# Kernel tuning notes

Measured on AMD Instinct MI355X. Metric: run time of the kernel, lower is better.

Reference implementation:

```python
import jax, jax.numpy as jnp
import numpy as np

M = 100   # memory_size
D = 512   # memory_dim
B, C, H, W = 4, 512, 64, 64
LN_EPS = 512.0  # nn.LayerNorm(300, 512): 2nd positional arg is eps (faithful quirk)


def _l2norm(x):
    # F.normalize(x, dim=1): x / max(||x||_2, 1e-12)
    return x / jnp.maximum(jnp.linalg.norm(x, axis=1, keepdims=True), 1e-12)


def setup_inputs() -> dict:
    key = jax.random.key(0)
    ks = jax.random.split(key, 16)
    s = 0.03  # weight scale to keep activations sane
    return {
        "fea":    jax.random.normal(ks[0], (B, C, H, W), jnp.float32),
        "item_w": jax.random.normal(ks[1], (D, D), jnp.float32) * 0.02,
        "rel_w":  jax.random.normal(ks[2], (M, D, D), jnp.float32) * 0.02,
        "W1": jax.random.normal(ks[3], (C, D), jnp.float32) * s,  "b1": jnp.zeros((D,), jnp.float32),
        "W2": jax.random.normal(ks[4], (C, D), jnp.float32) * s,  "b2": jnp.zeros((D,), jnp.float32),
        "W3": jax.random.normal(ks[5], (C, M), jnp.float32) * s,  "b3": jnp.zeros((M,), jnp.float32),
        "Wqkv": jax.random.normal(ks[6], (D, 3 * M), jnp.float32) * s, "bqkv": jnp.zeros((3 * M,), jnp.float32),
        "ln_g": jnp.ones((3 * M,), jnp.float32), "ln_b": jnp.zeros((3 * M,), jnp.float32),
        "Wr1": jax.random.normal(ks[7], (D * D, D), jnp.float32) * s, "br1": jnp.zeros((D,), jnp.float32),
        "Wr2": jax.random.normal(ks[8], (M * D, D), jnp.float32) * s, "br2": jnp.zeros((D,), jnp.float32),
    }


def reference(fea, item_w, rel_w, W1, b1, W2, b2, W3, b3,
              Wqkv, bqkv, ln_g, ln_b, Wr1, br1, Wr2, br2):
    b, c, h, w = fea.shape
    x = fea.transpose(0, 2, 3, 1).reshape(b * h * w, c)        # (N, C)
    qn = _l2norm(x)
    ip1 = qn @ W1 + b1                                          # (N, D)
    ip2 = qn @ W2 + b2                                          # (N, D)
    ip3 = jax.nn.softmax(qn @ W3 + b3, axis=-1)                 # (N, M)
    # ip4[b,f] = sum_{n,d} ip3[b,n] ip2[b,d] rel_w[n,d,f]; scan over the M
    # memory slots to avoid an (N, M, D) intermediate.
    def _slot(acc, nw):
        coef, Wn = nw                                           # (N,), (D, D)
        return acc + coef[:, None] * (ip2 @ Wn), None
    ip4, _ = jax.lax.scan(_slot, jnp.zeros_like(ip2), (ip3.T, rel_w))
    # einsum('bd,cf->df', ip4, ip2) == outer(sum_b ip4, sum_c ip2)
    item0 = jnp.outer(ip4.sum(0), ip2.sum(0))                   # (D, D)
    item1 = item_w + ip1.T @ ip1                                # (D, D)
    qkv = (item0 + 1.0 * item1) @ Wqkv + bqkv                   # alpha2=1.0, (D, 3M)
    mu = qkv.mean(-1, keepdims=True)
    var = jnp.var(qkv, axis=-1, keepdims=True)                  # biased, as torch LN
    qkv = (qkv - mu) / jnp.sqrt(var + LN_EPS) * ln_g + ln_b
    q, k, v = qkv[:, :M].T, qkv[:, M:2 * M].T, qkv[:, 2 * M:].T  # each (M, D)
    # op_att: rel0[i,d,f] = sum_j tanh(q[i,d]*k[j,d]) * v[j,f]
    t = jnp.tanh(q[:, None, :] * k[None, :, :])                 # (M, M, D)
    rel0 = jnp.einsum('ijd,jf->idf', t, v)                      # (M, D, D)
    rel_w_new = rel_w + 1.0 * rel0                              # alpha1=1.0
    memory = rel_w_new.reshape(M, D * D) @ Wr1 + br1            # (M, D)
    mn = _l2norm(memory)
    addr = jax.nn.softmax(qn @ mn.T, axis=1)                    # (N, M)
    mf = (addr @ mn).reshape(b, h, w, c).transpose(0, 3, 1, 2)  # (b, C, h, w)
    return jnp.concatenate([fea, mf], axis=1)                   # (b, 2C, h, w)
```

## Files before the change

### kernel.cpp

```cpp
#include <hip/hip_runtime.h>
#include <hip/hip_bf16.h>

#define NTOK 16384
#define DDIM 512
#define MMEM 100
#define HWSZ 4096
#define QKVW 300

typedef __attribute__((ext_vector_type(8))) short short8v;
typedef __attribute__((ext_vector_type(4))) short short4v;
typedef __attribute__((ext_vector_type(4))) float f32x4;

__device__ __forceinline__ unsigned short f2bf(float x) {
  union { __hip_bfloat16 h; unsigned short u; } cv;
  cv.h = __float2bfloat16(x);
  return cv.u;
}
__device__ __forceinline__ float bf2f(unsigned short u) {
  union { unsigned int u; float f; } v; v.u = ((unsigned int)u) << 16;
  return v.f;
}

__global__ __launch_bounds__(256) void feat_cvtw_k(
    const float* __restrict__ fea, unsigned short* __restrict__ qnbf,
    float* __restrict__ out,
    const float* __restrict__ W1, const float* __restrict__ W2,
    const float* __restrict__ W3, const float* __restrict__ Wq,
    const float* __restrict__ b1, const float* __restrict__ b2,
    unsigned short* __restrict__ Wcat, unsigned short* __restrict__ o3,
    unsigned short* __restrict__ oq, float* __restrict__ bcat) {
  if (blockIdx.x >= 512) {
    int base = (blockIdx.x - 512) * 256 + threadIdx.x;
    for (int idx = base; idx < 467968; idx += 229 * 256) {
      if (idx < 262144) {
        int k = idx >> 9, n = idx & 511;
        Wcat[(size_t)k * 1024 + n] = f2bf(W1[idx]);
        Wcat[(size_t)k * 1024 + 512 + n] = f2bf(W2[idx]);
      } else if (idx < 313344) {
        o3[idx - 262144] = f2bf(W3[idx - 262144]);
      } else if (idx < 466944) {
        oq[idx - 313344] = f2bf(Wq[idx - 313344]);
      } else {
        int i = idx - 466944;
        bcat[i] = (i < 512) ? b1[i] : b2[i - 512];
      }
    }
    return;
  }
  __shared__ float tile[512][33];
  __shared__ float psum[8][32];
  __shared__ float invn_s[32];
  const int bid = blockIdx.x;
  const int b = bid >> 7, hw0 = (bid & 127) * 32;
  const int t = threadIdx.x;
  const int hwo = t & 31, cg = t >> 5;
  const float* src = fea + (size_t)b * DDIM * HWSZ + hw0;
  float* dst = out + (size_t)b * (2 * DDIM) * HWSZ + hw0;
  float ss = 0.f;
#pragma unroll 8
  for (int i = 0; i < 64; ++i) {
    int c = cg * 64 + i;
    float v = src[(size_t)c * HWSZ + hwo];
    tile[c][hwo] = v;
    dst[(size_t)c * HWSZ + hwo] = v;
    ss += v * v;
  }
  psum[cg][hwo] = ss;
  __syncthreads();
  if (t < 32) {
    float s = 0.f;
#pragma unroll
    for (int j = 0; j < 8; ++j) s += psum[j][t];
    invn_s[t] = 1.f / fmaxf(sqrtf(s), 1e-12f);
  }
  __syncthreads();
  const int tok = t & 31, c0 = (t >> 5) * 64;
  const float inv = invn_s[tok];
  unsigned short* qp = qnbf + ((size_t)(b * HWSZ + hw0 + tok)) * DDIM + c0;
#pragma unroll
  for (int e8 = 0; e8 < 8; ++e8) {
    short8v p;
#pragma unroll
    for (int e = 0; e < 8; ++e)
      p[e] = (short)f2bf(tile[c0 + e8 * 8 + e][tok] * inv);
    *(short8v*)(qp + e8 * 8) = p;
  }
}

template<bool OUTBF>
__global__ __launch_bounds__(256) void gemm_bf16_k(
    const unsigned short* __restrict__ A, const unsigned short* __restrict__ B,
    const float* __restrict__ bias, void* __restrict__ Cv,
    int M, int N, int K, int lda, int ldb, int ldc) {
  __shared__ unsigned short As[128][40];
  __shared__ unsigned short Bs[32][132];
  const int tid = threadIdx.x;
  const int l = tid & 63, w = tid >> 6;
  const int l15 = l & 15, lhi = l >> 4;
  const int wm = w >> 1, wn = w & 1;
  const int row0 = blockIdx.y * 128, col0 = blockIdx.x * 128;
  const int am = tid >> 1, akq = (tid & 1) << 4;
  const int bk = tid >> 3, bnq = (tid & 7) << 4;
  const int arow = row0 + am;
  f32x4 acc[4][4] = {};

  for (int k0 = 0; k0 < K; k0 += 32) {
    short8v av0 = {}, av1 = {}, bv0 = {}, bv1 = {};
    if (arow < M && k0 + akq < K) {
      const unsigned short* ap = A + (size_t)arow * lda + k0 + akq;
      if (k0 + akq + 15 < K) {
        av0 = *(const short8v*)ap;
        av1 = *(const short8v*)(ap + 8);
      } else {
#pragma unroll
        for (int e = 0; e < 8; ++e) {
          av0[e] = (k0 + akq + e < K) ? (short)ap[e] : (short)0;
          av1[e] = (k0 + akq + 8 + e < K) ? (short)ap[8 + e] : (short)0;
        }
      }
    }
    {
      const int kk = k0 + bk;
      if (kk < K) {
        const unsigned short* bp = B + (size_t)kk * ldb + col0 + bnq;
        if (col0 + bnq + 15 < N) {
          bv0 = *(const short8v*)bp;
          bv1 = *(const short8v*)(bp + 8);
        } else {
#pragma unroll
          for (int e = 0; e < 8; ++e) {
            bv0[e] = (col0 + bnq + e < N) ? (short)bp[e] : (short)0;
            bv1[e] = (col0 + bnq + 8 + e < N) ? (short)bp[8 + e] : (short)0;
          }
        }
      }
    }
    __syncthreads();
    *(short8v*)&As[am][akq] = av0;
    *(short8v*)&As[am][akq + 8] = av1;
    *(short8v*)&Bs[bk][bnq] = bv0;
    *(short8v*)&Bs[bk][bnq + 8] = bv1;
    __syncthreads();
    short8v af[4];
#pragma unroll
    for (int mt = 0; mt < 4; ++mt)
      af[mt] = *(const short8v*)&As[wm * 64 + mt * 16 + l15][lhi * 8];
#pragma unroll
    for (int ct = 0; ct < 4; ++ct) {
      union { short8v v; unsigned short u[8]; } bf;
      const int nn = wn * 64 + ct * 16 + l15;
#pragma unroll
      for (int j = 0; j < 8; ++j) bf.u[j] = Bs[lhi * 8 + j][nn];
#pragma unroll
      for (int mt = 0; mt < 4; ++mt)
        acc[mt][ct] = __builtin_amdgcn_mfma_f32_16x16x32_bf16(
            af[mt], bf.v, acc[mt][ct], 0, 0, 0);
    }
  }

#pragma unroll
  for (int mt = 0; mt < 4; ++mt) {
    const int rb = row0 + wm * 64 + mt * 16 + lhi * 4;
#pragma unroll
    for (int u = 0; u < 4; ++u) {
      const int r = rb + u;
      if (r >= M) continue;
#pragma unroll
      for (int ct = 0; ct < 4; ++ct) {
        const int c = col0 + wn * 64 + ct * 16 + l15;
        if (c >= N) continue;
        float val = acc[mt][ct][u];
        if (bias) val += bias[c];
        if (OUTBF) ((unsigned short*)Cv)[(size_t)r * ldc + c] = f2bf(val);
        else       ((float*)Cv)[(size_t)r * ldc + c] = val;
      }
    }
  }
}

__global__ __launch_bounds__(256) void gemm_qkv_k(
    const float* __restrict__ item, const float* __restrict__ item_w,
    const float* __restrict__ s4, const float* __restrict__ s2,
    const unsigned short* __restrict__ B, const float* __restrict__ bias,
    float* __restrict__ C) {
  __shared__ unsigned short As[128][40];
  __shared__ unsigned short Bs[32][132];
  const int tid = threadIdx.x;
  const int l = tid & 63, w = tid >> 6;
  const int l15 = l & 15, lhi = l >> 4;
  const int wm = w >> 1, wn = w & 1;
  const int row0 = blockIdx.y * 128, col0 = blockIdx.x * 128;
  const int am = tid >> 1, akq = (tid & 1) << 4;
  const int bk = tid >> 3, bnq = (tid & 7) << 4;
  const int arow = row0 + am;
  f32x4 acc[4][4] = {};

  for (int k0 = 0; k0 < DDIM; k0 += 32) {
    float av[16];
    {
      const size_t off = (size_t)arow * DDIM + k0 + akq;
      const float s4r = s4[arow];
#pragma unroll
      for (int u = 0; u < 4; ++u) {
        float4 a = *(const float4*)(item + off + 4 * u);
        float4 b = *(const float4*)(item_w + off + 4 * u);
        float4 c = *(const float4*)(s2 + k0 + akq + 4 * u);
        av[4*u+0] = a.x + b.x + s4r * c.x;
        av[4*u+1] = a.y + b.y + s4r * c.y;
        av[4*u+2] = a.z + b.z + s4r * c.z;
        av[4*u+3] = a.w + b.w + s4r * c.w;
      }
    }
    short8v bv0 = {}, bv1 = {};
    {
      const int kk = k0 + bk;
      const unsigned short* bp = B + (size_t)kk * QKVW + col0 + bnq;
      if (col0 + bnq + 15 < QKVW) {
        bv0 = *(const short8v*)bp;
        bv1 = *(const short8v*)(bp + 8);
      } else {
#pragma unroll
        for (int e = 0; e < 8; ++e) {
          bv0[e] = (col0 + bnq + e < QKVW) ? (short)bp[e] : (short)0;
          bv1[e] = (col0 + bnq + 8 + e < QKVW) ? (short)bp[8 + e] : (short)0;
        }
      }
    }
    __syncthreads();
    {
      short8v p0, p1;
#pragma unroll
      for (int e = 0; e < 8; ++e) p0[e] = (short)f2bf(av[e]);
#pragma unroll
      for (int e = 0; e < 8; ++e) p1[e] = (short)f2bf(av[8 + e]);
      *(short8v*)&As[am][akq] = p0;
      *(short8v*)&As[am][akq + 8] = p1;
    }
    *(short8v*)&Bs[bk][bnq] = bv0;
    *(short8v*)&Bs[bk][bnq + 8] = bv1;
    __syncthreads();
    short8v af[4];
#pragma unroll
    for (int mt = 0; mt < 4; ++mt)
      af[mt] = *(const short8v*)&As[wm * 64 + mt * 16 + l15][lhi * 8];
#pragma unroll
    for (int ct = 0; ct < 4; ++ct) {
      union { short8v v; unsigned short u[8]; } bf;
      const int nn = wn * 64 + ct * 16 + l15;
#pragma unroll
      for (int j = 0; j < 8; ++j) bf.u[j] = Bs[lhi * 8 + j][nn];
#pragma unroll
      for (int mt = 0; mt < 4; ++mt)
        acc[mt][ct] = __builtin_amdgcn_mfma_f32_16x16x32_bf16(
            af[mt], bf.v, acc[mt][ct], 0, 0, 0);
    }
  }

#pragma unroll
  for (int mt = 0; mt < 4; ++mt) {
    const int rb = row0 + wm * 64 + mt * 16 + lhi * 4;
#pragma unroll
    for (int u = 0; u < 4; ++u) {
      const int r = rb + u;
#pragma unroll
      for (int ct = 0; ct < 4; ++ct) {
        const int c = col0 + wn * 64 + ct * 16 + l15;
        if (c >= QKVW) continue;
        C[(size_t)r * QKVW + c] = acc[mt][ct][u] + bias[c];
      }
    }
  }
}

__global__ __launch_bounds__(256) void gemm_sm100_k(
    const unsigned short* __restrict__ A, const unsigned short* __restrict__ B,
    const float* __restrict__ bias, unsigned short* __restrict__ obf,
    int lda, int ldb, int ldo) {
  __shared__ unsigned short As[128][40];
  __shared__ unsigned short Bs[32][132];
  __shared__ float Ps[128][104];
  const int tid = threadIdx.x;
  const int l = tid & 63, w = tid >> 6;
  const int l15 = l & 15, lhi = l >> 4;
  const int wm = w >> 1, wn = w & 1;
  const int row0 = blockIdx.x * 128;
  const int am = tid >> 1, akq = (tid & 1) << 4;
  const int bk = tid >> 3, bnq = (tid & 7) << 4;
  f32x4 acc[4][4] = {};

  for (int k0 = 0; k0 < DDIM; k0 += 32) {
    const unsigned short* ap = A + (size_t)(row0 + am) * lda + k0 + akq;
    short8v av0 = *(const short8v*)ap;
    short8v av1 = *(const short8v*)(ap + 8);
    short8v bv0 = {}, bv1 = {};
    const unsigned short* bp = B + (size_t)(k0 + bk) * ldb + bnq;
    if (bnq + 15 < MMEM) {
      bv0 = *(const short8v*)bp;
      bv1 = *(const short8v*)(bp + 8);
    } else {
#pragma unroll
      for (int e = 0; e < 8; ++e) {
        bv0[e] = (bnq + e < MMEM) ? (short)bp[e] : (short)0;
        bv1[e] = (bnq + 8 + e < MMEM) ? (short)bp[8 + e] : (short)0;
      }
    }
    __syncthreads();
    *(short8v*)&As[am][akq] = av0;
    *(short8v*)&As[am][akq + 8] = av1;
    *(short8v*)&Bs[bk][bnq] = bv0;
    *(short8v*)&Bs[bk][bnq + 8] = bv1;
    __syncthreads();
    short8v af[4];
#pragma unroll
    for (int mt = 0; mt < 4; ++mt)
      af[mt] = *(const short8v*)&As[wm * 64 + mt * 16 + l15][lhi * 8];
#pragma unroll
    for (int ct = 0; ct < 4; ++ct) {
      union { short8v v; unsigned short u[8]; } bf;
      const int nn = wn * 64 + ct * 16 + l15;
#pragma unroll
      for (int j = 0; j < 8; ++j) bf.u[j] = Bs[lhi * 8 + j][nn];
#pragma unroll
      for (int mt = 0; mt < 4; ++mt)
        acc[mt][ct] = __builtin_amdgcn_mfma_f32_16x16x32_bf16(
            af[mt], bf.v, acc[mt][ct], 0, 0, 0);
    }
  }

#pragma unroll
  for (int mt = 0; mt < 4; ++mt) {
#pragma unroll
    for (int u = 0; u < 4; ++u) {
      const int r = wm * 64 + mt * 16 + lhi * 4 + u;
#pragma unroll
      for (int ct = 0; ct < 4; ++ct) {
        const int c = wn * 64 + ct * 16 + l15;
        if (c < MMEM) {
          float val = acc[mt][ct][u];
          if (bias) val += bias[c];
          Ps[r][c] = val;
        }
      }
    }
  }
  __syncthreads();
  for (int rr = 0; rr < 32; ++rr) {
    const int r = w * 32 + rr;
    float v0 = Ps[r][l];
    const bool has1 = (l + 64) < MMEM;
    float v1 = has1 ? Ps[r][l + 64] : -3.4e38f;
    float m = fmaxf(v0, v1);
#pragma unroll
    for (int o = 32; o; o >>= 1) m = fmaxf(m, __shfl_xor(m, o, 64));
    float e0 = expf(v0 - m);
    float e1 = has1 ? expf(v1 - m) : 0.f;
    float s = e0 + e1;
#pragma unroll
    for (int o = 32; o; o >>= 1) s += __shfl_xor(s, o, 64);
    float inv = 1.f / s;
    unsigned short* orow = obf + (size_t)(row0 + r) * ldo;
    orow[l] = f2bf(e0 * inv);
    if (has1) orow[l + 64] = f2bf(e1 * inv);
  }
}

__global__ __launch_bounds__(256) void atb_bf16_k(
    const unsigned short* __restrict__ A, const unsigned short* __restrict__ B,
    float* __restrict__ C, int M, int N, int K,
    int lda, int ldb, int ldc, int KC) {
  __shared__ unsigned short As[128][40];
  __shared__ unsigned short Bs[32][132];
  const int tid = threadIdx.x;
  const int l = tid & 63, w = tid >> 6;
  const int l15 = l & 15, lhi = l >> 4;
  const int wm = w >> 1, wn = w & 1;
  const int row0 = blockIdx.y * 128, col0 = blockIdx.x * 128;
  const int kbeg = blockIdx.z * KC;
  const int kend = min(kbeg + KC, K);
  const int akk = tid >> 3, amq = (tid & 7) << 4;
  const int bk = tid >> 3, bnq = (tid & 7) << 4;
  f32x4 acc[4][4] = {};

  for (int k0 = kbeg; k0 < kend; k0 += 32) {
    unsigned short av[16]; short8v bv0 = {}, bv1 = {};
    {
      const int kk = k0 + akk;
      if (kk < kend) {
        const unsigned short* ap = A + (size_t)kk * lda + row0 + amq;
        if (row0 + amq + 15 < M) {
          *(short8v*)&av[0] = *(const short8v*)ap;
          *(short8v*)&av[8] = *(const short8v*)(ap + 8);
        } else {
#pragma unroll
          for (int e = 0; e < 16; ++e)
            av[e] = (row0 + amq + e < M) ? ap[e] : 0;
        }
      } else {
#pragma unroll
        for (int e = 0; e < 16; ++e) av[e] = 0;
      }
    }
    {
      const int kk = k0 + bk;
      if (kk < kend) {
        const unsigned short* bp = B + (size_t)kk * ldb + col0 + bnq;
        if (col0 + bnq + 15 < N) {
          bv0 = *(const short8v*)bp;
          bv1 = *(const short8v*)(bp + 8);
        } else {
#pragma unroll
          for (int e = 0; e < 8; ++e) {
            bv0[e] = (col0 + bnq + e < N) ? (short)bp[e] : (short)0;
            bv1[e] = (col0 + bnq + 8 + e < N) ? (short)bp[8 + e] : (short)0;
          }
        }
      }
    }
    __syncthreads();
#pragma unroll
    for (int e = 0; e < 16; ++e) As[amq + e][akk] = av[e];
    *(short8v*)&Bs[bk][bnq] = bv0;
    *(short8v*)&Bs[bk][bnq + 8] = bv1;
    __syncthreads();
    short8v af[4];
#pragma unroll
    for (int mt = 0; mt < 4; ++mt)
      af[mt] = *(const short8v*)&As[wm * 64 + mt * 16 + l15][lhi * 8];
#pragma unroll
    for (int ct = 0; ct < 4; ++ct) {
      union { short8v v; unsigned short u[8]; } bf;
      const int nn = wn * 64 + ct * 16 + l15;
#pragma unroll
      for (int j = 0; j < 8; ++j) bf.u[j] = Bs[lhi * 8 + j][nn];
#pragma unroll
      for (int mt = 0; mt < 4; ++mt)
        acc[mt][ct] = __builtin_amdgcn_mfma_f32_16x16x32_bf16(
            af[mt], bf.v, acc[mt][ct], 0, 0, 0);
    }
  }

#pragma unroll
  for (int mt = 0; mt < 4; ++mt) {
    const int rb = row0 + wm * 64 + mt * 16 + lhi * 4;
#pragma unroll
    for (int u = 0; u < 4; ++u) {
      const int r = rb + u;
      if (r >= M) continue;
#pragma unroll
      for (int ct = 0; ct < 4; ++ct) {
        const int c = col0 + wn * 64 + ct * 16 + l15;
        if (c >= N) continue;
        atomicAdd(&C[(size_t)r * ldc + c], acc[mt][ct][u]);
      }
    }
  }
}

__global__ __launch_bounds__(256) void rel0_mfma_k(
    const float* __restrict__ qm, const float* __restrict__ km,
    const float* __restrict__ vm, const float* __restrict__ rel_w,
    unsigned short* __restrict__ relbf) {
  __shared__ unsigned short Ts[128][136];
  __shared__ unsigned short Vs[128][136];
  __shared__ float qv[128];
  const int i = blockIdx.y;
  const int d0 = blockIdx.x * 128;
  const int tid = threadIdx.x;
  const int l = tid & 63, w = tid >> 6;
  const int l15 = l & 15, lhi = l >> 4;
  const int wm = w >> 1, wn = w & 1;

  if (tid < 128) qv[tid] = qm[(size_t)i * DDIM + d0 + tid];
  __syncthreads();
#pragma unroll
  for (int p = 0; p < 8; ++p) {
    int g = p * 2048 + tid * 8;
    int j = g >> 7, dd = g & 127;
    if (j < MMEM) {
      const float* kp = km + (size_t)j * DDIM + d0 + dd;
      float4 k0v = *(const float4*)kp;
      float4 k1v = *(const float4*)(kp + 4);
      float kv[8] = {k0v.x, k0v.y, k0v.z, k0v.w, k1v.x, k1v.y, k1v.z, k1v.w};
#pragma unroll
      for (int e = 0; e < 8; ++e)
        Ts[dd + e][j] = f2bf(tanhf(qv[dd + e] * kv[e]));
    } else {
#pragma unroll
      for (int e = 0; e < 8; ++e) Ts[dd + e][j] = 0;
    }
  }

  for (int f0 = 0; f0 < DDIM; f0 += 128) {
    __syncthreads();
#pragma unroll
    for (int p = 0; p < 8; ++p) {
      int g = p * 2048 + tid * 8;
      int j = g >> 7, ff = g & 127;
      short8v pv;
      if (j < MMEM) {
        const float* vp = vm + (size_t)j * DDIM + f0 + ff;
        float4 v0 = *(const float4*)vp;
        float4 v1 = *(const float4*)(vp + 4);
        pv[0] = (short)f2bf(v0.x); pv[1] = (short)f2bf(v0.y);
        pv[2] = (short)f2bf(v0.z); pv[3] = (short)f2bf(v0.w);
        pv[4] = (short)f2bf(v1.x); pv[5] = (short)f2bf(v1.y);
        pv[6] = (short)f2bf(v1.z); pv[7] = (short)f2bf(v1.w);
      } else {
#pragma unroll
        for (int e = 0; e < 8; ++e) pv[e] = 0;
      }
      *(short8v*)&Vs[j][ff] = pv;
    }
    __syncthreads();
    f32x4 acc[4][4] = {};
#pragma unroll
    for (int ks = 0; ks < 4; ++ks) {
      const int kb = ks * 32;
      short8v af[4];
#pragma unroll
      for (int mt = 0; mt < 4; ++mt)
        af[mt] = *(const short8v*)&Ts[wm * 64 + mt * 16 + l15][kb + lhi * 8];
#pragma unroll
      for (int ct = 0; ct < 4; ++ct) {
        union { short8v v; unsigned short u[8]; } bf;
        const int nn = wn * 64 + ct * 16 + l15;
#pragma unroll
        for (int jj = 0; jj < 8; ++jj) bf.u[jj] = Vs[kb + lhi * 8 + jj][nn];
#pragma unroll
        for (int mt = 0; mt < 4; ++mt)
          acc[mt][ct] = __builtin_amdgcn_mfma_f32_16x16x32_bf16(
              af[mt], bf.v, acc[mt][ct], 0, 0, 0);
      }
    }
#pragma unroll
    for (int mt = 0; mt < 4; ++mt) {
#pragma unroll
      for (int u = 0; u < 4; ++u) {
        const int d = d0 + wm * 64 + mt * 16 + lhi * 4 + u;
        const size_t base = (size_t)i * 262144 + (size_t)d * DDIM;
#pragma unroll
        for (int ct = 0; ct < 4; ++ct) {
          const int f = f0 + wn * 64 + ct * 16 + l15;
          relbf[base + f] = f2bf(rel_w[base + f] + acc[mt][ct][u]);
        }
      }
    }
  }
}

#define MGK 262144
#define MGKC 1024
#define MGCHUNK 256
__global__ __launch_bounds__(1024, 4) void memgemm_k(
    const unsigned short* __restrict__ Ag, const float* __restrict__ Bg,
    float* __restrict__ partial) {
  __shared__ unsigned short As[128][44];
  __shared__ unsigned short Bs[32][520];
  const int tid = threadIdx.x;
  const int l = tid & 63, w = tid >> 6;
  const int l15 = l & 15, lhi = l >> 4;
  const int kbeg = blockIdx.x * MGKC;
  const int arow = tid >> 3, akq = tid & 7;
  const int bk = tid >> 5, bnq = (tid & 31) * 16;
  const int bsw = ((bk >> 3) & 3) << 4;
  const int csw = lhi << 4;
  f32x4 acc[8][2] = {};

  for (int t32 = 0; t32 < MGKC / 32; ++t32) {
    const int kb = kbeg + t32 * 32;
    short4v av = {};
    if (arow < MMEM)
      av = *(const short4v*)(Ag + (size_t)arow * MGK + kb + akq * 4);
    float4 bv[4];
    const float* bp = Bg + (size_t)(kb + bk) * DDIM + bnq;
#pragma unroll
    for (int u = 0; u < 4; ++u) bv[u] = *(const float4*)(bp + 4 * u);
    __syncthreads();
    *(short4v*)&As[arow][akq * 4] = av;
#pragma unroll
    for (int u = 0; u < 2; ++u) {
      short8v pb;
      pb[0] = (short)f2bf(bv[2*u].x);   pb[1] = (short)f2bf(bv[2*u].y);
      pb[2] = (short)f2bf(bv[2*u].z);   pb[3] = (short)f2bf(bv[2*u].w);
      pb[4] = (short)f2bf(bv[2*u+1].x); pb[5] = (short)f2bf(bv[2*u+1].y);
      pb[6] = (short)f2bf(bv[2*u+1].z); pb[7] = (short)f2bf(bv[2*u+1].w);
      *(short8v*)&Bs[bk][(bnq + u * 8) ^ bsw] = pb;
    }
    __syncthreads();
    union { short8v v; unsigned short u[8]; } bf0, bf1;
    const int nn0 = w * 32 + l15, nn1 = w * 32 + 16 + l15;
#pragma unroll
    for (int j = 0; j < 8; ++j) {
      bf0.u[j] = Bs[lhi * 8 + j][nn0 ^ csw];
      bf1.u[j] = Bs[lhi * 8 + j][nn1 ^ csw];
    }
#pragma unroll
    for (int mt = 0; mt < 8; ++mt) {
      short8v af = *(const short8v*)&As[mt * 16 + l15][lhi * 8];
      acc[mt][0] = __builtin_amdgcn_mfma_f32_16x16x32_bf16(af, bf0.v, acc[mt][0], 0, 0, 0);
      acc[mt][1] = __builtin_amdgcn_mfma_f32_16x16x32_bf16(af, bf1.v, acc[mt][1], 0, 0, 0);
    }
  }

  float* pw = partial + (size_t)blockIdx.x * (MMEM * DDIM);
#pragma unroll
  for (int mt = 0; mt < 8; ++mt) {
    const int r0 = mt * 16 + lhi * 4;
#pragma unroll
    for (int r = 0; r < 4; ++r) {
      const int row = r0 + r;
      if (row < MMEM) {
        pw[(size_t)row * DDIM + w * 32 + l15]      = acc[mt][0][r];
        pw[(size_t)row * DDIM + w * 32 + 16 + l15] = acc[mt][1][r];
      }
    }
  }
}

__global__ __launch_bounds__(512) void reduce_mn_k(
    const float* __restrict__ partial, const float* __restrict__ br1,
    unsigned short* __restrict__ mnbf, unsigned short* __restrict__ mnTbf) {
  __shared__ float r1[8];
  const int i = blockIdx.x, t = threadIdx.x;
  const float* p = partial + (size_t)i * DDIM + t;
  float a0 = 0.f, a1 = 0.f, a2 = 0.f, a3 = 0.f;
  float a4 = 0.f, a5 = 0.f, a6 = 0.f, a7 = 0.f;
  const size_t zs = (size_t)(MMEM * DDIM);
  for (int z = 0; z < MGCHUNK; z += 8) {
    a0 += p[(z + 0) * zs]; a1 += p[(z + 1) * zs];
    a2 += p[(z + 2) * zs]; a3 += p[(z + 3) * zs];
    a4 += p[(z + 4) * zs]; a5 += p[(z + 5) * zs];
    a6 += p[(z + 6) * zs]; a7 += p[(z + 7) * zs];
  }
  float a = br1[t] + ((a0 + a1) + (a2 + a3)) + ((a4 + a5) + (a6 + a7));
  float q = a * a;
#pragma unroll
  for (int o = 32; o; o >>= 1) q += __shfl_xor(q, o, 64);
  if ((t & 63) == 0) r1[t >> 6] = q;
  __syncthreads();
  q = 0.f;
#pragma unroll
  for (int j = 0; j < 8; ++j) q += r1[j];
  float inv = 1.f / fmaxf(sqrtf(q), 1e-12f);
  unsigned short hv = f2bf(a * inv);
  mnbf[(size_t)i * DDIM + t] = hv;
  mnTbf[(size_t)t * MMEM + i] = hv;
}

__global__ __launch_bounds__(512) void colsum_bf_k(const unsigned short* __restrict__ A,
                                                   int ld, float* __restrict__ out) {
  int d = threadIdx.x;
  const unsigned short* p = A + (size_t)blockIdx.x * 64 * ld + d;
  float a0 = 0.f, a1 = 0.f, a2 = 0.f, a3 = 0.f;
  for (int r = 0; r < 64; r += 4) {
    a0 += bf2f(p[(size_t)(r + 0) * ld]);
    a1 += bf2f(p[(size_t)(r + 1) * ld]);
    a2 += bf2f(p[(size_t)(r + 2) * ld]);
    a3 += bf2f(p[(size_t)(r + 3) * ld]);
  }
  atomicAdd(&out[d], (a0 + a1) + (a2 + a3));
}

__global__ __launch_bounds__(256) void ip4sum_k(const float* __restrict__ S,
                                                const float* __restrict__ rel_w,
                                                float* __restrict__ out) {
  __shared__ float sv[64];
  int r0 = blockIdx.x * 64;
  int tid = threadIdx.x;
  if (tid < 64) sv[tid] = S[r0 + tid];
  __syncthreads();
  float a0 = 0.f, a1 = 0.f, a2 = 0.f, a3 = 0.f;
  float b0 = 0.f, b1 = 0.f, b2 = 0.f, b3 = 0.f;
  const float* base = rel_w + (size_t)r0 * DDIM;
  for (int r = 0; r < 64; r += 4) {
    const float* p0 = base + (size_t)(r + 0) * DDIM;
    const float* p1 = base + (size_t)(r + 1) * DDIM;
    const float* p2 = base + (size_t)(r + 2) * DDIM;
    const float* p3 = base + (size_t)(r + 3) * DDIM;
    a0 = fmaf(sv[r + 0], p0[tid], a0); b0 = fmaf(sv[r + 0], p0[tid + 256], b0);
    a1 = fmaf(sv[r + 1], p1[tid], a1); b1 = fmaf(sv[r + 1], p1[tid + 256], b1);
    a2 = fmaf(sv[r + 2], p2[tid], a2); b2 = fmaf(sv[r + 2], p2[tid + 256], b2);
    a3 = fmaf(sv[r + 3], p3[tid], a3); b3 = fmaf(sv[r + 3], p3[tid + 256], b3);
  }
  atomicAdd(&out[tid], (a0 + a1) + (a2 + a3));
  atomicAdd(&out[tid + 256], (b0 + b1) + (b2 + b3));
}

__global__ __launch_bounds__(256) void ln300_k(const float* __restrict__ x,
                                               const float* __restrict__ g,
                                               const float* __restrict__ bb,
                                               float* __restrict__ qm,
                                               float* __restrict__ km,
                                               float* __restrict__ vm) {
  __shared__ float r1[4], r2[4];
  int row = blockIdx.x, tid = threadIdx.x;
  const float* xr = x + (size_t)row * QKVW;
  float v1 = xr[tid];
  float v2 = (tid + 256 < QKVW) ? xr[tid + 256] : 0.f;
  float s = v1 + v2, q = v1 * v1 + v2 * v2;
#pragma unroll
  for (int o = 32; o; o >>= 1) { s += __shfl_xor(s, o, 64); q += __shfl_xor(q, o, 64); }
  if ((tid & 63) == 0) { r1[tid >> 6] = s; r2[tid >> 6] = q; }
  __syncthreads();
  s = r1[0] + r1[1] + r1[2] + r1[3];
  q = r2[0] + r2[1] + r2[2] + r2[3];
  float mean = s * (1.f / 300.f);
  float var = q * (1.f / 300.f) - mean * mean;
  float inv = rsqrtf(var + 512.0f);
  float y1 = (v1 - mean) * inv * g[tid] + bb[tid];
  int j = tid;
  if (j < 100)      qm[(size_t)j * DDIM + row] = y1;
  else if (j < 200) km[(size_t)(j - 100) * DDIM + row] = y1;
  else              vm[(size_t)(j - 200) * DDIM + row] = y1;
  if (tid + 256 < QKVW) {
    float y2 = (v2 - mean) * inv * g[tid + 256] + bb[tid + 256];
    vm[(size_t)(tid + 56) * DDIM + row] = y2;
  }
}

__global__ void write_mf_k(const unsigned short* __restrict__ mfbf,
                           float* __restrict__ out) {
  __shared__ float tile[32][33];
  int b = blockIdx.z, hw0 = blockIdx.x * 32, c0 = blockIdx.y * 32;
  int tx = threadIdx.x, ty = threadIdx.y;
#pragma unroll
  for (int i = 0; i < 32; i += 8)
    tile[ty + i][tx] =
        bf2f(mfbf[((size_t)b * HWSZ + hw0 + ty + i) * DDIM + c0 + tx]);
  __syncthreads();
#pragma unroll
  for (int i = 0; i < 32; i += 8)
    out[(size_t)b * 4194304 + (size_t)(512 + c0 + ty + i) * HWSZ + hw0 + tx] =
        tile[tx][ty + i];
}

extern "C" void kernel_launch(void* const* d_in, const int* in_sizes, int n_in,
                              void* d_out, int out_size, void* d_ws, size_t ws_size,
                              hipStream_t stream) {
  (void)in_sizes; (void)n_in; (void)out_size; (void)ws_size;
  const float* fea    = (const float*)d_in[0];
  const float* item_w = (const float*)d_in[1];
  const float* rel_w  = (const float*)d_in[2];
  const float* W1     = (const float*)d_in[3];
  const float* b1     = (const float*)d_in[4];
  const float* W2     = (const float*)d_in[5];
  const float* b2     = (const float*)d_in[6];
  const float* W3     = (const float*)d_in[7];
  const float* b3     = (const float*)d_in[8];
  const float* Wqkv   = (const float*)d_in[9];
  const float* bqkv   = (const float*)d_in[10];
  const float* ln_g   = (const float*)d_in[11];
  const float* ln_b   = (const float*)d_in[12];
  const float* Wr1    = (const float*)d_in[13];
  const float* br1    = (const float*)d_in[14];
  float* out = (float*)d_out;
  float* ws = (float*)d_ws;

  float* S       = ws;
  float* ip4sum  = S       + 51200;
  float* ip2sum  = ip4sum  + 512;
  float* item    = ip2sum  + 512;
  float* qkv     = item    + 262144;
  float* qm      = qkv     + 153600;
  float* km      = qm      + 51200;
  float* vm      = km      + 51200;
  float* bcat    = vm      + 51200;
  float* partial = bcat    + 1024;
  unsigned short* u16base = (unsigned short*)(partial + 13107200);
  unsigned short* qnbf    = u16base;
  unsigned short* ip12bf  = qnbf    + 8388608;
  unsigned short* ip3bf   = ip12bf  + 16777216;
  unsigned short* addrbf  = ip3bf   + 1638400;
  unsigned short* relbf   = addrbf  + 2097152;
  unsigned short* mfbf    = relbf   + 26214400;
  unsigned short* mnbf    = mfbf    + 8388608;
  unsigned short* mnTbf   = mnbf    + 51200;
  unsigned short* Wcat    = mnTbf   + 51200;
  unsigned short* W3bf    = Wcat    + 524288;
  unsigned short* Wqbf    = W3bf    + 51200;

  hipMemsetAsync(S, 0, (size_t)(51200 + 512 + 512 + 262144) * sizeof(float), stream);

  feat_cvtw_k<<<741, 256, 0, stream>>>(fea, qnbf, out, W1, W2, W3, Wqkv,
                                       b1, b2, Wcat, W3bf, Wqbf, bcat);

  gemm_bf16_k<true><<<dim3(8, 128), 256, 0, stream>>>(
      qnbf, Wcat, bcat, ip12bf, NTOK, 1024, DDIM, DDIM, 1024, 1024);
  gemm_sm100_k<<<128, 256, 0, stream>>>(qnbf, W3bf, b3, ip3bf, DDIM, MMEM, MMEM);

  atb_bf16_k<<<dim3(4, 4, 32), 256, 0, stream>>>(
      ip12bf, ip12bf, item, DDIM, DDIM, NTOK, 1024, 1024, DDIM, 512);
  atb_bf16_k<<<dim3(4, 1, 64), 256, 0, stream>>>(
      ip3bf, ip12bf + 512, S, MMEM, DDIM, NTOK, MMEM, 1024, DDIM, 256);
  colsum_bf_k<<<256, 512, 0, stream>>>(ip12bf + 512, 1024, ip2sum);
  ip4sum_k<<<800, 256, 0, stream>>>(S, rel_w, ip4sum);

  gemm_qkv_k<<<dim3(3, 4), 256, 0, stream>>>(item, item_w, ip4sum, ip2sum,
                                             Wqbf, bqkv, qkv);
  ln300_k<<<512, 256, 0, stream>>>(qkv, ln_g, ln_b, qm, km, vm);

  rel0_mfma_k<<<dim3(4, MMEM), 256, 0, stream>>>(qm, km, vm, rel_w, relbf);

  memgemm_k<<<dim3(MGCHUNK), 1024, 0, stream>>>(relbf, Wr1, partial);
  reduce_mn_k<<<MMEM, 512, 0, stream>>>(partial, br1, mnbf, mnTbf);

  gemm_sm100_k<<<128, 256, 0, stream>>>(qnbf, mnTbf, nullptr, addrbf, DDIM, MMEM, 128);
  gemm_bf16_k<true><<<dim3(4, 128), 256, 0, stream>>>(
      addrbf, mnbf, nullptr, mfbf, NTOK, DDIM, MMEM, 128, DDIM, DDIM);

  write_mf_k<<<dim3(128, 16, 4), dim3(32, 8), 0, stream>>>(mfbf, out);
}
```

Measured before the change: 554.4 us.

## Merge independent GEMM launches and fuse mf GEMM with transposed output write

Combines the ip1/ip2 GEMM and the ip3 softmax GEMM into one launch that dispatches on block index. It also merges the two A^T·B reductions and the ip2 column sum into a single launch. The final addr@mn GEMM now writes transposed fp32 results straight into the output through shared memory, which removes the bf16 mf intermediate and the separate transpose kernel. The sm100 softmax staging buffer is switched to bf16 and aliased over the tile buffers to shrink shared memory. The aim is to cut launch count, tail bubbles and an extra global round trip. The cost is extra rounding of logits to bf16 before the softmax.

```diff
diff --git a/kernel.cpp b/kernel.cpp
--- a/kernel.cpp
+++ b/kernel.cpp
@@ -87,18 +87,18 @@
   }
 }
 
-template<bool OUTBF>
-__global__ __launch_bounds__(256) void gemm_bf16_k(
-    const unsigned short* __restrict__ A, const unsigned short* __restrict__ B,
-    const float* __restrict__ bias, void* __restrict__ Cv,
-    int M, int N, int K, int lda, int ldb, int ldc) {
-  __shared__ unsigned short As[128][40];
-  __shared__ unsigned short Bs[32][132];
+__device__ __forceinline__ void gemm_body(
+    char* smem, const unsigned short* __restrict__ A,
+    const unsigned short* __restrict__ B, const float* __restrict__ bias,
+    unsigned short* __restrict__ Cbf,
+    int M, int N, int K, int lda, int ldb, int ldc, int bx, int by) {
+  unsigned short (*As)[40] = (unsigned short(*)[40])smem;
+  unsigned short (*Bs)[132] = (unsigned short(*)[132])(smem + 10240);
   const int tid = threadIdx.x;
   const int l = tid & 63, w = tid >> 6;
   const int l15 = l & 15, lhi = l >> 4;
   const int wm = w >> 1, wn = w & 1;
-  const int row0 = blockIdx.y * 128, col0 = blockIdx.x * 128;
+  const int row0 = by * 128, col0 = bx * 128;
   const int am = tid >> 1, akq = (tid & 1) << 4;
   const int bk = tid >> 3, bnq = (tid & 7) << 4;
   const int arow = row0 + am;
@@ -171,10 +171,333 @@
         if (c >= N) continue;
         float val = acc[mt][ct][u];
         if (bias) val += bias[c];
-        if (OUTBF) ((unsigned short*)Cv)[(size_t)r * ldc + c] = f2bf(val);
-        else       ((float*)Cv)[(size_t)r * ldc + c] = val;
-      }
-    }
+        Cbf[(size_t)r * ldc + c] = f2bf(val);
+      }
+    }
+  }
+}
+
+__device__ __forceinline__ void sm100_body(
+    char* smem, const unsigned short* __restrict__ A,
+    const unsigned short* __restrict__ B, const float* __restrict__ bias,
+    unsigned short* __restrict__ obf, int lda, int ldb, int ldo, int rowblk) {
+  unsigned short (*As)[40] = (unsigned short(*)[40])smem;
+  unsigned short (*Bs)[132] = (unsigned short(*)[132])(smem + 10240);
+  unsigned short (*Ps)[104] = (unsigned short(*)[104])smem;
+  const int tid = threadIdx.x;
+  const int l = tid & 63, w = tid >> 6;
+  const int l15 = l & 15, lhi = l >> 4;
+  const int wm = w >> 1, wn = w & 1;
+  const int row0 = rowblk * 128;
+  const int am = tid >> 1, akq = (tid & 1) << 4;
+  const int bk = tid >> 3, bnq = (tid & 7) << 4;
+  f32x4 acc[4][4] = {};
+
+  for (int k0 = 0; k0 < DDIM; k0 += 32) {
+    const unsigned short* ap = A + (size_t)(row0 + am) * lda + k0 + akq;
+    short8v av0 = *(const short8v*)ap;
+    short8v av1 = *(const short8v*)(ap + 8);
+    short8v bv0 = {}, bv1 = {};
+    const unsigned short* bp = B + (size_t)(k0 + bk) * ldb + bnq;
+    if (bnq + 15 < MMEM) {
+      bv0 = *(const short8v*)bp;
+      bv1 = *(const short8v*)(bp + 8);
+    } else {
+#pragma unroll
+      for (int e = 0; e < 8; ++e) {
+        bv0[e] = (bnq + e < MMEM) ? (short)bp[e] : (short)0;
+        bv1[e] = (bnq + 8 + e < MMEM) ? (short)bp[8 + e] : (short)0;
+      }
+    }
+    __syncthreads();
+    *(short8v*)&As[am][akq] = av0;
+    *(short8v*)&As[am][akq + 8] = av1;
+    *(short8v*)&Bs[bk][bnq] = bv0;
+    *(short8v*)&Bs[bk][bnq + 8] = bv1;
+    __syncthreads();
+    short8v af[4];
+#pragma unroll
+    for (int mt = 0; mt < 4; ++mt)
+      af[mt] = *(const short8v*)&As[wm * 64 + mt * 16 + l15][lhi * 8];
+#pragma unroll
+    for (int ct = 0; ct < 4; ++ct) {
+      union { short8v v; unsigned short u[8]; } bf;
+      const int nn = wn * 64 + ct * 16 + l15;
+#pragma unroll
+      for (int j = 0; j < 8; ++j) bf.u[j] = Bs[lhi * 8 + j][nn];
+#pragma unroll
+      for (int mt = 0; mt < 4; ++mt)
+        acc[mt][ct] = __builtin_amdgcn_mfma_f32_16x16x32_bf16(
+            af[mt], bf.v, acc[mt][ct], 0, 0, 0);
+    }
+  }
+
+  __syncthreads();
+#pragma unroll
+  for (int mt = 0; mt < 4; ++mt) {
+#pragma unroll
+    for (int u = 0; u < 4; ++u) {
+      const int r = wm * 64 + mt * 16 + lhi * 4 + u;
+#pragma unroll
+      for (int ct = 0; ct < 4; ++ct) {
+        const int c = wn * 64 + ct * 16 + l15;
+        if (c < MMEM) {
+          float val = acc[mt][ct][u];
+          if (bias) val += bias[c];
+          Ps[r][c] = f2bf(val);
+        }
+      }
+    }
+  }
+  __syncthreads();
+  for (int rr = 0; rr < 32; ++rr) {
+    const int r = w * 32 + rr;
+    float v0 = bf2f(Ps[r][l]);
+    const bool has1 = (l + 64) < MMEM;
+    float v1 = has1 ? bf2f(Ps[r][l + 64]) : -3.4e38f;
+    float m = fmaxf(v0, v1);
+#pragma unroll
+    for (int o = 32; o; o >>= 1) m = fmaxf(m, __shfl_xor(m, o, 64));
+    float e0 = expf(v0 - m);
+    float e1 = has1 ? expf(v1 - m) : 0.f;
+    float s = e0 + e1;
+#pragma unroll
+    for (int o = 32; o; o >>= 1) s += __shfl_xor(s, o, 64);
+    float inv = 1.f / s;
+    unsigned short* orow = obf + (size_t)(row0 + r) * ldo;
+    orow[l] = f2bf(e0 * inv);
+    if (has1) orow[l + 64] = f2bf(e1 * inv);
+  }
+}
+
+__device__ __forceinline__ void atb_body(
+    char* smem, const unsigned short* __restrict__ A,
+    const unsigned short* __restrict__ B, float* __restrict__ C,
+    int M, int N, int K, int lda, int ldb, int ldc, int KC,
+    int bx, int by, int bz) {
+  unsigned short (*As)[40] = (unsigned short(*)[40])smem;
+  unsigned short (*Bs)[132] = (unsigned short(*)[132])(smem + 10240);
+  const int tid = threadIdx.x;
+  const int l = tid & 63, w = tid >> 6;
+  const int l15 = l & 15, lhi = l >> 4;
+  const int wm = w >> 1, wn = w & 1;
+  const int row0 = by * 128, col0 = bx * 128;
+  const int kbeg = bz * KC;
+  const int kend = min(kbeg + KC, K);
+  const int akk = tid >> 3, amq = (tid & 7) << 4;
+  const int bk = tid >> 3, bnq = (tid & 7) << 4;
+  f32x4 acc[4][4] = {};
+
+  for (int k0 = kbeg; k0 < kend; k0 += 32) {
+    unsigned short av[16]; short8v bv0 = {}, bv1 = {};
+    {
+      const int kk = k0 + akk;
+      if (kk < kend) {
+        const unsigned short* ap = A + (size_t)kk * lda + row0 + amq;
+        if (row0 + amq + 15 < M) {
+          *(short8v*)&av[0] = *(const short8v*)ap;
+          *(short8v*)&av[8] = *(const short8v*)(ap + 8);
+        } else {
+#pragma unroll
+          for (int e = 0; e < 16; ++e)
+            av[e] = (row0 + amq + e < M) ? ap[e] : 0;
+        }
+      } else {
+#pragma unroll
+        for (int e = 0; e < 16; ++e) av[e] = 0;
+      }
+    }
+    {
+      const int kk = k0 + bk;
+      if (kk < kend) {
+        const unsigned short* bp = B + (size_t)kk * ldb + col0 + bnq;
+        if (col0 + bnq + 15 < N) {
+          bv0 = *(const short8v*)bp;
+          bv1 = *(const short8v*)(bp + 8);
+        } else {
+#pragma unroll
+          for (int e = 0; e < 8; ++e) {
+            bv0[e] = (col0 + bnq + e < N) ? (short)bp[e] : (short)0;
+            bv1[e] = (col0 + bnq + 8 + e < N) ? (short)bp[8 + e] : (short)0;
+          }
+        }
+      }
+    }
+    __syncthreads();
+#pragma unroll
+    for (int e = 0; e < 16; ++e) As[amq + e][akk] = av[e];
+    *(short8v*)&Bs[bk][bnq] = bv0;
+    *(short8v*)&Bs[bk][bnq + 8] = bv1;
+    __syncthreads();
+    short8v af[4];
+#pragma unroll
+    for (int mt = 0; mt < 4; ++mt)
+      af[mt] = *(const short8v*)&As[wm * 64 + mt * 16 + l15][lhi * 8];
+#pragma unroll
+    for (int ct = 0; ct < 4; ++ct) {
+      union { short8v v; unsigned short u[8]; } bf;
+      const int nn = wn * 64 + ct * 16 + l15;
+#pragma unroll
+      for (int j = 0; j < 8; ++j) bf.u[j] = Bs[lhi * 8 + j][nn];
+#pragma unroll
+      for (int mt = 0; mt < 4; ++mt)
+        acc[mt][ct] = __builtin_amdgcn_mfma_f32_16x16x32_bf16(
+            af[mt], bf.v, acc[mt][ct], 0, 0, 0);
+    }
+  }
+
+#pragma unroll
+  for (int mt = 0; mt < 4; ++mt) {
+    const int rb = row0 + wm * 64 + mt * 16 + lhi * 4;
+#pragma unroll
+    for (int u = 0; u < 4; ++u) {
+      const int r = rb + u;
+      if (r >= M) continue;
+#pragma unroll
+      for (int ct = 0; ct < 4; ++ct) {
+        const int c = col0 + wn * 64 + ct * 16 + l15;
+        if (c >= N) continue;
+        atomicAdd(&C[(size_t)r * ldc + c], acc[mt][ct][u]);
+      }
+    }
+  }
+}
+
+__global__ __launch_bounds__(256) void step2_k(
+    const unsigned short* __restrict__ qnbf, const unsigned short* __restrict__ Wcat,
+    const float* __restrict__ bcat, unsigned short* __restrict__ ip12bf,
+    const unsigned short* __restrict__ W3bf, const float* __restrict__ b3,
+    unsigned short* __restrict__ ip3bf) {
+  __shared__ char smem[26624];
+  const int bid = blockIdx.x;
+  if (bid < 1024) {
+    gemm_body(smem, qnbf, Wcat, bcat, ip12bf, NTOK, 1024, DDIM,
+              DDIM, 1024, 1024, bid & 7, bid >> 3);
+  } else {
+    sm100_body(smem, qnbf, W3bf, b3, ip3bf, DDIM, MMEM, MMEM, bid - 1024);
+  }
+}
+
+__global__ __launch_bounds__(256) void step3_k(
+    const unsigned short* __restrict__ ip12bf, const unsigned short* __restrict__ ip3bf,
+    float* __restrict__ item, float* __restrict__ S, float* __restrict__ ip2sum) {
+  __shared__ char smem[18688];
+  const int bid = blockIdx.x;
+  const int t = threadIdx.x;
+  if (bid < 512) {
+    atb_body(smem, ip12bf, ip12bf, item, DDIM, DDIM, NTOK,
+             1024, 1024, DDIM, 512, bid & 3, (bid >> 2) & 3, bid >> 4);
+  } else if (bid < 768) {
+    const int b2 = bid - 512;
+    atb_body(smem, ip3bf, ip12bf + 512, S, MMEM, DDIM, NTOK,
+             MMEM, 1024, DDIM, 256, b2 & 3, 0, b2 >> 2);
+  } else {
+    const int cb = bid - 768;
+    const unsigned short* p = ip12bf + 512 + (size_t)cb * 64 * 1024 + t;
+    float a0 = 0.f, a1 = 0.f, a2 = 0.f, a3 = 0.f;
+    float b0 = 0.f, b1 = 0.f, b2 = 0.f, b3 = 0.f;
+    for (int r = 0; r < 64; r += 4) {
+      a0 += bf2f(p[(size_t)(r + 0) * 1024]); b0 += bf2f(p[(size_t)(r + 0) * 1024 + 256]);
+      a1 += bf2f(p[(size_t)(r + 1) * 1024]); b1 += bf2f(p[(size_t)(r + 1) * 1024 + 256]);
+      a2 += bf2f(p[(size_t)(r + 2) * 1024]); b2 += bf2f(p[(size_t)(r + 2) * 1024 + 256]);
+      a3 += bf2f(p[(size_t)(r + 3) * 1024]); b3 += bf2f(p[(size_t)(r + 3) * 1024 + 256]);
+    }
+    atomicAdd(&ip2sum[t], (a0 + a1) + (a2 + a3));
+    atomicAdd(&ip2sum[t + 256], (b0 + b1) + (b2 + b3));
+  }
+}
+
+__global__ __launch_bounds__(256) void sm100_addr_k(
+    const unsigned short* __restrict__ qnbf, const unsigned short* __restrict__ mnTbf,
+    unsigned short* __restrict__ addrbf) {
+  __shared__ char smem[26624];
+  sm100_body(smem, qnbf, mnTbf, nullptr, addrbf, DDIM, MMEM, 128, blockIdx.x);
+}
+
+__global__ __launch_bounds__(256) void gemm_mf_out_k(
+    const unsigned short* __restrict__ A, const unsigned short* __restrict__ B,
+    float* __restrict__ out) {
+  __shared__ char smem[35328];
+  unsigned short (*As)[40] = (unsigned short(*)[40])smem;
+  unsigned short (*Bs)[132] = (unsigned short(*)[132])(smem + 10240);
+  unsigned short (*Ps)[138] = (unsigned short(*)[138])smem;
+  const int tid = threadIdx.x;
+  const int l = tid & 63, w = tid >> 6;
+  const int l15 = l & 15, lhi = l >> 4;
+  const int wm = w >> 1, wn = w & 1;
+  const int row0 = blockIdx.y * 128, col0 = blockIdx.x * 128;
+  const int am = tid >> 1, akq = (tid & 1) << 4;
+  const int bk = tid >> 3, bnq = (tid & 7) << 4;
+  const int K = MMEM, lda = 128, ldb = DDIM;
+  f32x4 acc[4][4] = {};
+
+  for (int k0 = 0; k0 < 128; k0 += 32) {
+    short8v av0 = {}, av1 = {}, bv0 = {}, bv1 = {};
+    if (k0 + akq < K) {
+      const unsigned short* ap = A + (size_t)(row0 + am) * lda + k0 + akq;
+      if (k0 + akq + 15 < K) {
+        av0 = *(const short8v*)ap;
+        av1 = *(const short8v*)(ap + 8);
+      } else {
+#pragma unroll
+        for (int e = 0; e < 8; ++e) {
+          av0[e] = (k0 + akq + e < K) ? (short)ap[e] : (short)0;
+          av1[e] = (k0 + akq + 8 + e < K) ? (short)ap[8 + e] : (short)0;
+        }
+      }
+    }
+    {
+      const int kk = k0 + bk;
+      if (kk < K) {
+        const unsigned short* bp = B + (size_t)kk * ldb + col0 + bnq;
+        bv0 = *(const short8v*)bp;
+        bv1 = *(const short8v*)(bp + 8);
+      }
+    }
+    __syncthreads();
+    *(short8v*)&As[am][akq] = av0;
+    *(short8v*)&As[am][akq + 8] = av1;
+    *(short8v*)&Bs[bk][bnq] = bv0;
+    *(short8v*)&Bs[bk][bnq + 8] = bv1;
+    __syncthreads();
+    short8v af[4];
+#pragma unroll
+    for (int mt = 0; mt < 4; ++mt)
+      af[mt] = *(const short8v*)&As[wm * 64 + mt * 16 + l15][lhi * 8];
+#pragma unroll
+    for (int ct = 0; ct < 4; ++ct) {
+      union { short8v v; unsigned short u[8]; } bf;
+      const int nn = wn * 64 + ct * 16 + l15;
+#pragma unroll
+      for (int j = 0; j < 8; ++j) bf.u[j] = Bs[lhi * 8 + j][nn];
+#pragma unroll
+      for (int mt = 0; mt < 4; ++mt)
+        acc[mt][ct] = __builtin_amdgcn_mfma_f32_16x16x32_bf16(
+            af[mt], bf.v, acc[mt][ct], 0, 0, 0);
+    }
+  }
+
+  __syncthreads();
+#pragma unroll
+  for (int mt = 0; mt < 4; ++mt) {
+#pragma unroll
+    for (int u = 0; u < 4; ++u) {
+      const int r = wm * 64 + mt * 16 + lhi * 4 + u;
+#pragma unroll
+      for (int ct = 0; ct < 4; ++ct) {
+        const int c = wn * 64 + ct * 16 + l15;
+        Ps[r][c] = f2bf(acc[mt][ct][u]);
+      }
+    }
+  }
+  __syncthreads();
+  const int b = row0 >> 12;
+  const int hwb = row0 & 4095;
+  const int j = tid & 63;
+  float* obase = out + (size_t)b * 4194304 + (size_t)(512 + col0) * HWSZ + hwb;
+  for (int cr = tid >> 6; cr < 128; cr += 4) {
+    obase[(size_t)cr * HWSZ + j]      = bf2f(Ps[j][cr]);
+    obase[(size_t)cr * HWSZ + j + 64] = bf2f(Ps[j + 64][cr]);
   }
 }
 
@@ -267,190 +590,6 @@
         const int c = col0 + wn * 64 + ct * 16 + l15;
         if (c >= QKVW) continue;
         C[(size_t)r * QKVW + c] = acc[mt][ct][u] + bias[c];
-      }
-    }
-  }
-}
-
-__global__ __launch_bounds__(256) void gemm_sm100_k(
-    const unsigned short* __restrict__ A, const unsigned short* __restrict__ B,
-    const float* __restrict__ bias, unsigned short* __restrict__ obf,
-    int lda, int ldb, int ldo) {
-  __shared__ unsigned short As[128][40];
-  __shared__ unsigned short Bs[32][132];
-  __shared__ float Ps[128][104];
-  const int tid = threadIdx.x;
-  const int l = tid & 63, w = tid >> 6;
-  const int l15 = l & 15, lhi = l >> 4;
-  const int wm = w >> 1, wn = w & 1;
-  const int row0 = blockIdx.x * 128;
-  const int am = tid >> 1, akq = (tid & 1) << 4;
-  const int bk = tid >> 3, bnq = (tid & 7) << 4;
-  f32x4 acc[4][4] = {};
-
-  for (int k0 = 0; k0 < DDIM; k0 += 32) {
-    const unsigned short* ap = A + (size_t)(row0 + am) * lda + k0 + akq;
-    short8v av0 = *(const short8v*)ap;
-    short8v av1 = *(const short8v*)(ap + 8);
-    short8v bv0 = {}, bv1 = {};
-    const unsigned short* bp = B + (size_t)(k0 + bk) * ldb + bnq;
-    if (bnq + 15 < MMEM) {
-      bv0 = *(const short8v*)bp;
-      bv1 = *(const short8v*)(bp + 8);
-    } else {
-#pragma unroll
-      for (int e = 0; e < 8; ++e) {
-        bv0[e] = (bnq + e < MMEM) ? (short)bp[e] : (short)0;
-        bv1[e] = (bnq + 8 + e < MMEM) ? (short)bp[8 + e] : (short)0;
-      }
-    }
-    __syncthreads();
-    *(short8v*)&As[am][akq] = av0;
-    *(short8v*)&As[am][akq + 8] = av1;
-    *(short8v*)&Bs[bk][bnq] = bv0;
-    *(short8v*)&Bs[bk][bnq + 8] = bv1;
-    __syncthreads();
-    short8v af[4];
-#pragma unroll
-    for (int mt = 0; mt < 4; ++mt)
-      af[mt] = *(const short8v*)&As[wm * 64 + mt * 16 + l15][lhi * 8];
-#pragma unroll
-    for (int ct = 0; ct < 4; ++ct) {
-      union { short8v v; unsigned short u[8]; } bf;
-      const int nn = wn * 64 + ct * 16 + l15;
-#pragma unroll
-      for (int j = 0; j < 8; ++j) bf.u[j] = Bs[lhi * 8 + j][nn];
-#pragma unroll
-      for (int mt = 0; mt < 4; ++mt)
-        acc[mt][ct] = __builtin_amdgcn_mfma_f32_16x16x32_bf16(
-            af[mt], bf.v, acc[mt][ct], 0, 0, 0);
-    }
-  }
-
-#pragma unroll
-  for (int mt = 0; mt < 4; ++mt) {
-#pragma unroll
-    for (int u = 0; u < 4; ++u) {
-      const int r = wm * 64 + mt * 16 + lhi * 4 + u;
-#pragma unroll
-      for (int ct = 0; ct < 4; ++ct) {
-        const int c = wn * 64 + ct * 16 + l15;
-        if (c < MMEM) {
-          float val = acc[mt][ct][u];
-          if (bias) val += bias[c];
-          Ps[r][c] = val;
-        }
-      }
-    }
-  }
-  __syncthreads();
-  for (int rr = 0; rr < 32; ++rr) {
-    const int r = w * 32 + rr;
-    float v0 = Ps[r][l];
-    const bool has1 = (l + 64) < MMEM;
-    float v1 = has1 ? Ps[r][l + 64] : -3.4e38f;
-    float m = fmaxf(v0, v1);
-#pragma unroll
-    for (int o = 32; o; o >>= 1) m = fmaxf(m, __shfl_xor(m, o, 64));
-    float e0 = expf(v0 - m);
-    float e1 = has1 ? expf(v1 - m) : 0.f;
-    float s = e0 + e1;
-#pragma unroll
-    for (int o = 32; o; o >>= 1) s += __shfl_xor(s, o, 64);
-    float inv = 1.f / s;
-    unsigned short* orow = obf + (size_t)(row0 + r) * ldo;
-    orow[l] = f2bf(e0 * inv);
-    if (has1) orow[l + 64] = f2bf(e1 * inv);
-  }
-}
-
-__global__ __launch_bounds__(256) void atb_bf16_k(
-    const unsigned short* __restrict__ A, const unsigned short* __restrict__ B,
-    float* __restrict__ C, int M, int N, int K,
-    int lda, int ldb, int ldc, int KC) {
-  __shared__ unsigned short As[128][40];
-  __shared__ unsigned short Bs[32][132];
-  const int tid = threadIdx.x;
-  const int l = tid & 63, w = tid >> 6;
-  const int l15 = l & 15, lhi = l >> 4;
-  const int wm = w >> 1, wn = w & 1;
-  const int row0 = blockIdx.y * 128, col0 = blockIdx.x * 128;
-  const int kbeg = blockIdx.z * KC;
-  const int kend = min(kbeg + KC, K);
-  const int akk = tid >> 3, amq = (tid & 7) << 4;
-  const int bk = tid >> 3, bnq = (tid & 7) << 4;
-  f32x4 acc[4][4] = {};
-
-  for (int k0 = kbeg; k0 < kend; k0 += 32) {
-    unsigned short av[16]; short8v bv0 = {}, bv1 = {};
-    {
-      const int kk = k0 + akk;
-      if (kk < kend) {
-        const unsigned short* ap = A + (size_t)kk * lda + row0 + amq;
-        if (row0 + amq + 15 < M) {
-          *(short8v*)&av[0] = *(const short8v*)ap;
-          *(short8v*)&av[8] = *(const short8v*)(ap + 8);
-        } else {
-#pragma unroll
-          for (int e = 0; e < 16; ++e)
-            av[e] = (row0 + amq + e < M) ? ap[e] : 0;
-        }
-      } else {
-#pragma unroll
-        for (int e = 0; e < 16; ++e) av[e] = 0;
-      }
-    }
-    {
-      const int kk = k0 + bk;
-      if (kk < kend) {
-        const unsigned short* bp = B + (size_t)kk * ldb + col0 + bnq;
-        if (col0 + bnq + 15 < N) {
-          bv0 = *(const short8v*)bp;
-          bv1 = *(const short8v*)(bp + 8);
-        } else {
-#pragma unroll
-          for (int e = 0; e < 8; ++e) {
-            bv0[e] = (col0 + bnq + e < N) ? (short)bp[e] : (short)0;
-            bv1[e] = (col0 + bnq + 8 + e < N) ? (short)bp[8 + e] : (short)0;
-          }
-        }
-      }
-    }
-    __syncthreads();
-#pragma unroll
-    for (int e = 0; e < 16; ++e) As[amq + e][akk] = av[e];
-    *(short8v*)&Bs[bk][bnq] = bv0;
-    *(short8v*)&Bs[bk][bnq + 8] = bv1;
-    __syncthreads();
-    short8v af[4];
-#pragma unroll
-    for (int mt = 0; mt < 4; ++mt)
-      af[mt] = *(const short8v*)&As[wm * 64 + mt * 16 + l15][lhi * 8];
-#pragma unroll
-    for (int ct = 0; ct < 4; ++ct) {
-      union { short8v v; unsigned short u[8]; } bf;
-      const int nn = wn * 64 + ct * 16 + l15;
-#pragma unroll
-      for (int j = 0; j < 8; ++j) bf.u[j] = Bs[lhi * 8 + j][nn];
-#pragma unroll
-      for (int mt = 0; mt < 4; ++mt)
-        acc[mt][ct] = __builtin_amdgcn_mfma_f32_16x16x32_bf16(
-            af[mt], bf.v, acc[mt][ct], 0, 0, 0);
-    }
-  }
-
-#pragma unroll
-  for (int mt = 0; mt < 4; ++mt) {
-    const int rb = row0 + wm * 64 + mt * 16 + lhi * 4;
-#pragma unroll
-    for (int u = 0; u < 4; ++u) {
-      const int r = rb + u;
-      if (r >= M) continue;
-#pragma unroll
-      for (int ct = 0; ct < 4; ++ct) {
-        const int c = col0 + wn * 64 + ct * 16 + l15;
-        if (c >= N) continue;
-        atomicAdd(&C[(size_t)r * ldc + c], acc[mt][ct][u]);
       }
     }
   }
@@ -645,20 +784,6 @@
   unsigned short hv = f2bf(a * inv);
   mnbf[(size_t)i * DDIM + t] = hv;
   mnTbf[(size_t)t * MMEM + i] = hv;
-}
-
-__global__ __launch_bounds__(512) void colsum_bf_k(const unsigned short* __restrict__ A,
-                                                   int ld, float* __restrict__ out) {
-  int d = threadIdx.x;
-  const unsigned short* p = A + (size_t)blockIdx.x * 64 * ld + d;
-  float a0 = 0.f, a1 = 0.f, a2 = 0.f, a3 = 0.f;
-  for (int r = 0; r < 64; r += 4) {
-    a0 += bf2f(p[(size_t)(r + 0) * ld]);
-    a1 += bf2f(p[(size_t)(r + 1) * ld]);
-    a2 += bf2f(p[(size_t)(r + 2) * ld]);
-    a3 += bf2f(p[(size_t)(r + 3) * ld]);
-  }
-  atomicAdd(&out[d], (a0 + a1) + (a2 + a3));
 }
 
 __global__ __launch_bounds__(256) void ip4sum_k(const float* __restrict__ S,
@@ -716,22 +841,6 @@
     float y2 = (v2 - mean) * inv * g[tid + 256] + bb[tid + 256];
     vm[(size_t)(tid + 56) * DDIM + row] = y2;
   }
-}
-
-__global__ void write_mf_k(const unsigned short* __restrict__ mfbf,
-                           float* __restrict__ out) {
-  __shared__ float tile[32][33];
-  int b = blockIdx.z, hw0 = blockIdx.x * 32, c0 = blockIdx.y * 32;
-  int tx = threadIdx.x, ty = threadIdx.y;
-#pragma unroll
-  for (int i = 0; i < 32; i += 8)
-    tile[ty + i][tx] =
-        bf2f(mfbf[((size_t)b * HWSZ + hw0 + ty + i) * DDIM + c0 + tx]);
-  __syncthreads();
-#pragma unroll
-  for (int i = 0; i < 32; i += 8)
-    out[(size_t)b * 4194304 + (size_t)(512 + c0 + ty + i) * HWSZ + hw0 + tx] =
-        tile[tx][ty + i];
 }
 
 extern "C" void kernel_launch(void* const* d_in, const int* in_sizes, int n_in,
@@ -772,8 +881,7 @@
   unsigned short* ip3bf   = ip12bf  + 16777216;
   unsigned short* addrbf  = ip3bf   + 1638400;
   unsigned short* relbf   = addrbf  + 2097152;
-  unsigned short* mfbf    = relbf   + 26214400;
-  unsigned short* mnbf    = mfbf    + 8388608;
+  unsigned short* mnbf    = relbf   + 26214400;
   unsigned short* mnTbf   = mnbf    + 51200;
   unsigned short* Wcat    = mnTbf   + 51200;
   unsigned short* W3bf    = Wcat    + 524288;
@@ -784,15 +892,10 @@
   feat_cvtw_k<<<741, 256, 0, stream>>>(fea, qnbf, out, W1, W2, W3, Wqkv,
                                        b1, b2, Wcat, W3bf, Wqbf, bcat);
 
-  gemm_bf16_k<true><<<dim3(8, 128), 256, 0, stream>>>(
-      qnbf, Wcat, bcat, ip12bf, NTOK, 1024, DDIM, DDIM, 1024, 1024);
-  gemm_sm100_k<<<128, 256, 0, stream>>>(qnbf, W3bf, b3, ip3bf, DDIM, MMEM, MMEM);
-
-  atb_bf16_k<<<dim3(4, 4, 32), 256, 0, stream>>>(
-      ip12bf, ip12bf, item, DDIM, DDIM, NTOK, 1024, 1024, DDIM, 512);
-  atb_bf16_k<<<dim3(4, 1, 64), 256, 0, stream>>>(
-      ip3bf, ip12bf + 512, S, MMEM, DDIM, NTOK, MMEM, 1024, DDIM, 256);
-  colsum_bf_k<<<256, 512, 0, stream>>>(ip12bf + 512, 1024, ip2sum);
+  step2_k<<<1152, 256, 0, stream>>>(qnbf, Wcat, bcat, ip12bf, W3bf, b3, ip3bf);
+
+  step3_k<<<1024, 256, 0, stream>>>(ip12bf, ip3bf, item, S, ip2sum);
+
   ip4sum_k<<<800, 256, 0, stream>>>(S, rel_w, ip4sum);
 
   gemm_qkv_k<<<dim3(3, 4), 256, 0, stream>>>(item, item_w, ip4sum, ip2sum,
@@ -804,9 +907,6 @@
   memgemm_k<<<dim3(MGCHUNK), 1024, 0, stream>>>(relbf, Wr1, partial);
   reduce_mn_k<<<MMEM, 512, 0, stream>>>(partial, br1, mnbf, mnTbf);
 
-  gemm_sm100_k<<<128, 256, 0, stream>>>(qnbf, mnTbf, nullptr, addrbf, DDIM, MMEM, 128);
-  gemm_bf16_k<true><<<dim3(4, 128), 256, 0, stream>>>(
-      addrbf, mnbf, nullptr, mfbf, NTOK, DDIM, MMEM, 128, DDIM, DDIM);
-
-  write_mf_k<<<dim3(128, 16, 4), dim3(32, 8), 0, stream>>>(mfbf, out);
-}
+  sm100_addr_k<<<128, 256, 0, stream>>>(qnbf, mnTbf, addrbf);
+  gemm_mf_out_k<<<dim3(4, 128), 256, 0, stream>>>(addrbf, mnbf, out);
+}
```

Measured after the change: 503.4 us. 1.1x faster.
